# Kernel tuning notes

Hardware: AMD Instinct MI355X
Metric: run time of the kernel (lower is better)

## Reference

```python
import jax, jax.numpy as jnp
import numpy as np

B, N, IN_F = 2, 512, 10
SET_FEATS = [128, 128, 64]
HIDDEN = 256
D2 = 2 * SET_FEATS[-1]


def _init_linear(key, fout, fin):
    kw, kb = jax.random.split(key)
    bound = 1.0 / np.sqrt(fin)
    W = jax.random.uniform(kw, (fout, fin), jnp.float32, -bound, bound)
    b = jax.random.uniform(kb, (fout,), jnp.float32, -bound, bound)
    return W, b


def setup_inputs() -> dict:
    key = jax.random.key(0)
    keys = jax.random.split(key, 6)
    x = jax.random.normal(keys[0], (B, N, IN_F), jnp.float32)
    Ws0, bs0 = _init_linear(keys[1], SET_FEATS[0], IN_F)
    Ws1, bs1 = _init_linear(keys[2], SET_FEATS[1], SET_FEATS[0])
    Ws2, bs2 = _init_linear(keys[3], SET_FEATS[2], SET_FEATS[1])
    Wp0, bp0 = _init_linear(keys[4], HIDDEN, D2)
    Wp1, bp1 = _init_linear(keys[5], 1, HIDDEN)
    return {"x": x, "Ws0": Ws0, "bs0": bs0, "Ws1": Ws1, "bs1": bs1,
            "Ws2": Ws2, "bs2": bs2, "Wp0": Wp0, "bp0": bp0,
            "Wp1": Wp1, "bp1": bp1}


def reference(x, Ws0, bs0, Ws1, bs1, Ws2, bs2, Wp0, bp0, Wp1, bp1):
    # x: [B, N, in_features] -> transpose(2,1) -> [B, C, N]
    u = jnp.transpose(x, (0, 2, 1))
    # set_model: per-point MLP (1x1 conv stack), ReLU after each layer
    for W, b in ((Ws0, bs0), (Ws1, bs1), (Ws2, bs2)):
        u = jax.nn.relu(jnp.einsum('fc,bcn->bfn', W, u) + b[None, :, None])
    # pairwise block: cat([u_j broadcast, u_i broadcast], dim=1) -> [B, 2d, N, N]
    # fused into the first suffix 1x1 conv: out[b,f,i,j] = Wa@u[:,j] + Wb@u[:,i] + b
    d = Wp0.shape[1] // 2
    Wa, Wb = Wp0[:, :d], Wp0[:, d:]
    ha = jnp.einsum('fc,bcn->bfn', Wa, u)  # depends on j (m1[b,c,i,j] = u[b,c,j])
    hb = jnp.einsum('fc,bcn->bfn', Wb, u)  # depends on i (m2[b,c,i,j] = u[b,c,i])
    h = jax.nn.relu(ha[:, :, None, :] + hb[:, :, :, None] + bp0[None, :, None, None])
    # final 1x1 conv to 1 channel, no activation
    out = jnp.einsum('fc,bcij->bfij', Wp1, h) + bp1[None, :, None, None]
    return out  # [B, 1, N, N]
```

## Files before the change

kernel.cpp:

```cpp
#include <hip/hip_runtime.h>

#define BB 2
#define NN 512
#define INF 10
#define TI 64
#define TJ 32
#define FCH 128

static __device__ __forceinline__ float dot4(float4 w, float4 v, float acc) {
    acc = fmaf(w.x, v.x, acc);
    acc = fmaf(w.y, v.y, acc);
    acc = fmaf(w.z, v.z, acc);
    acc = fmaf(w.w, v.w, acc);
    return acc;
}

__global__ __launch_bounds__(256) void k_points(
    const float* __restrict__ x,
    const float* __restrict__ Ws0, const float* __restrict__ bs0,
    const float* __restrict__ Ws1, const float* __restrict__ bs1,
    const float* __restrict__ Ws2, const float* __restrict__ bs2,
    const float* __restrict__ Wp0, const float* __restrict__ bp0,
    float* __restrict__ haT, float* __restrict__ hbT)
{
    __shared__ __align__(16) float xs[4][INF];
    __shared__ __align__(16) float u0s[4][128];
    __shared__ __align__(16) float u1s[4][128];
    __shared__ __align__(16) float u2s[4][64];

    const int t  = threadIdx.x;
    const int p0 = blockIdx.x * 4;

    if (t < 4 * INF) {
        int p = t / INF, c = t % INF;
        xs[p][c] = x[(p0 + p) * INF + c];
    }
    __syncthreads();

    {
        const int f = t & 127, ph = t >> 7;
        float a0 = bs0[f], a1 = a0;
        #pragma unroll
        for (int c = 0; c < INF; ++c) {
            float w = Ws0[f * INF + c];
            a0 = fmaf(w, xs[ph * 2 + 0][c], a0);
            a1 = fmaf(w, xs[ph * 2 + 1][c], a1);
        }
        u0s[ph * 2 + 0][f] = fmaxf(a0, 0.f);
        u0s[ph * 2 + 1][f] = fmaxf(a1, 0.f);
    }
    __syncthreads();

    {
        const int f = t & 127, ph = t >> 7;
        float a0 = bs1[f], a1 = a0;
        const float4* wv = (const float4*)(Ws1 + f * 128);
        #pragma unroll 8
        for (int c4 = 0; c4 < 32; ++c4) {
            float4 w  = wv[c4];
            float4 x0 = *(const float4*)&u0s[ph * 2 + 0][c4 * 4];
            float4 x1 = *(const float4*)&u0s[ph * 2 + 1][c4 * 4];
            a0 = dot4(w, x0, a0);
            a1 = dot4(w, x1, a1);
        }
        u1s[ph * 2 + 0][f] = fmaxf(a0, 0.f);
        u1s[ph * 2 + 1][f] = fmaxf(a1, 0.f);
    }
    __syncthreads();

    {
        const int f = t & 63, p = t >> 6;
        float a = bs2[f];
        const float4* wv = (const float4*)(Ws2 + f * 128);
        #pragma unroll 8
        for (int c4 = 0; c4 < 32; ++c4) {
            float4 w  = wv[c4];
            float4 xv = *(const float4*)&u1s[p][c4 * 4];
            a = dot4(w, xv, a);
        }
        u2s[p][f] = fmaxf(a, 0.f);
    }
    __syncthreads();

    {
        const int f = t;
        float ah[4], bh[4];
        const float bb = bp0[f];
        #pragma unroll
        for (int p = 0; p < 4; ++p) { ah[p] = 0.f; bh[p] = bb; }
        const float4* wv = (const float4*)(Wp0 + f * 128);
        #pragma unroll 4
        for (int c4 = 0; c4 < 16; ++c4) {
            float4 wa = wv[c4];
            float4 wb = wv[16 + c4];
            #pragma unroll
            for (int p = 0; p < 4; ++p) {
                float4 u = *(const float4*)&u2s[p][c4 * 4];
                ah[p] = dot4(wa, u, ah[p]);
                bh[p] = dot4(wb, u, bh[p]);
            }
        }
        #pragma unroll
        for (int p = 0; p < 4; ++p) {
            haT[(size_t)(p0 + p) * 256 + f] = ah[p];
            hbT[(size_t)(p0 + p) * 256 + f] = bh[p];
        }
    }
}

__global__ __launch_bounds__(256) void k_outer(
    const float* __restrict__ haT, const float* __restrict__ hbT,
    const float* __restrict__ Wp1, const float* __restrict__ bp1,
    float* __restrict__ out)
{
    __shared__ __align__(512) float sA[TJ * FCH];
    __shared__ __align__(512) float sB[TI * FCH];

    const int t  = threadIdx.x;
    const int jb = blockIdx.x * TJ;
    const int ib = blockIdx.y * TI;
    const int b  = blockIdx.z;

    const int lane = t & 63, w = t >> 6;
    const int lj = lane & 15;
    const int li = lane >> 4;
    const int j0 = lj * 2;
    const int i0 = w * 16 + li * 4;
    const int xa = lj;
    const int xb = w * 4 + li;

    const uintptr_t aB0 = (uintptr_t)sA + (size_t)j0 * (FCH * 4) + (xa << 4);
    const uintptr_t aB1 = aB0 + FCH * 4;
    uintptr_t bBs[4];
    #pragma unroll
    for (int di = 0; di < 4; ++di)
        bBs[di] = (uintptr_t)sB + (size_t)(i0 + di) * (FCH * 4) + (xb << 4);

    float acc[4][2];
    #pragma unroll
    for (int di = 0; di < 4; ++di) { acc[di][0] = 0.f; acc[di][1] = 0.f; }

    const int sp = t & 31;

    for (int ph = 0; ph < 2; ++ph) {
        const int f0 = ph * FCH;
        if (ph) __syncthreads();

        #pragma unroll
        for (int k = 0; k < 4; ++k) {
            const int r  = (t >> 5) + 8 * k;
            const int sg = sp ^ ((r >> 1) & 15);
            float4 v = *(const float4*)(haT + ((size_t)(b * NN + jb + r)) * 256 + f0 + sg * 4);
            *(float4*)&sA[r * FCH + sp * 4] = v;
        }
        #pragma unroll
        for (int k = 0; k < 8; ++k) {
            const int r  = (t >> 5) + 8 * k;
            const int sg = sp ^ ((r >> 2) & 15);
            float4 v = *(const float4*)(hbT + ((size_t)(b * NN + ib + r)) * 256 + f0 + sg * 4);
            *(float4*)&sB[r * FCH + sp * 4] = v;
        }
        __syncthreads();

        const float4* wg = (const float4*)(Wp1 + f0);

        #pragma unroll 8
        for (int g = 0; g < 32; ++g) {
            const float4 w4 = wg[g];
            const uintptr_t gx = (uintptr_t)(g << 4);
            const float4 a0 = *(const float4*)(aB0 ^ gx);
            const float4 a1 = *(const float4*)(aB1 ^ gx);
            float4 bv[4];
            #pragma unroll
            for (int di = 0; di < 4; ++di) bv[di] = *(const float4*)(bBs[di] ^ gx);

            #pragma unroll
            for (int di = 0; di < 4; ++di) {
                acc[di][0] = fmaf(w4.x, fmaxf(a0.x + bv[di].x, 0.f), acc[di][0]);
                acc[di][1] = fmaf(w4.x, fmaxf(a1.x + bv[di].x, 0.f), acc[di][1]);
                acc[di][0] = fmaf(w4.y, fmaxf(a0.y + bv[di].y, 0.f), acc[di][0]);
                acc[di][1] = fmaf(w4.y, fmaxf(a1.y + bv[di].y, 0.f), acc[di][1]);
                acc[di][0] = fmaf(w4.z, fmaxf(a0.z + bv[di].z, 0.f), acc[di][0]);
                acc[di][1] = fmaf(w4.z, fmaxf(a1.z + bv[di].z, 0.f), acc[di][1]);
                acc[di][0] = fmaf(w4.w, fmaxf(a0.w + bv[di].w, 0.f), acc[di][0]);
                acc[di][1] = fmaf(w4.w, fmaxf(a1.w + bv[di].w, 0.f), acc[di][1]);
            }
        }
    }

    const float bias = bp1[0];
    float* o = out + (size_t)b * NN * NN;
    #pragma unroll
    for (int di = 0; di < 4; ++di) {
        float2 v = { acc[di][0] + bias, acc[di][1] + bias };
        *(float2*)&o[(size_t)(ib + i0 + di) * NN + (jb + j0)] = v;
    }
}

extern "C" void kernel_launch(void* const* d_in, const int* in_sizes, int n_in,
                              void* d_out, int out_size, void* d_ws, size_t ws_size,
                              hipStream_t stream) {
    const float* x   = (const float*)d_in[0];
    const float* Ws0 = (const float*)d_in[1];
    const float* bs0 = (const float*)d_in[2];
    const float* Ws1 = (const float*)d_in[3];
    const float* bs1 = (const float*)d_in[4];
    const float* Ws2 = (const float*)d_in[5];
    const float* bs2 = (const float*)d_in[6];
    const float* Wp0 = (const float*)d_in[7];
    const float* bp0 = (const float*)d_in[8];
    const float* Wp1 = (const float*)d_in[9];
    const float* bp1 = (const float*)d_in[10];

    float* haT = (float*)d_ws;
    float* hbT = haT + (size_t)BB * NN * 256;

    k_points<<<dim3(BB * NN / 4), dim3(256), 0, stream>>>(
        x, Ws0, bs0, Ws1, bs1, Ws2, bs2, Wp0, bp0, haT, hbT);

    k_outer<<<dim3(NN / TJ, NN / TI, BB), dim3(256), 0, stream>>>(
        haT, hbT, Wp1, bp1, (float*)d_out);
}
```

Before: 108.7 us.

## Prefetch second feature half into registers and use index-based swizzled LDS addressing

```diff
diff --git a/kernel.cpp b/kernel.cpp
--- a/kernel.cpp
+++ b/kernel.cpp
@@ -129,50 +129,59 @@
     const int xa = lj;
     const int xb = w * 4 + li;
 
-    const uintptr_t aB0 = (uintptr_t)sA + (size_t)j0 * (FCH * 4) + (xa << 4);
-    const uintptr_t aB1 = aB0 + FCH * 4;
-    uintptr_t bBs[4];
-    #pragma unroll
-    for (int di = 0; di < 4; ++di)
-        bBs[di] = (uintptr_t)sB + (size_t)(i0 + di) * (FCH * 4) + (xb << 4);
+    const int aOff0 = j0 * FCH;
+    const int aOff1 = aOff0 + FCH;
+    const int bOff0 = i0 * FCH;
 
     float acc[4][2];
     #pragma unroll
     for (int di = 0; di < 4; ++di) { acc[di][0] = 0.f; acc[di][1] = 0.f; }
 
     const int sp = t & 31;
-
-    for (int ph = 0; ph < 2; ++ph) {
-        const int f0 = ph * FCH;
-        if (ph) __syncthreads();
-
-        #pragma unroll
-        for (int k = 0; k < 4; ++k) {
-            const int r  = (t >> 5) + 8 * k;
-            const int sg = sp ^ ((r >> 1) & 15);
-            float4 v = *(const float4*)(haT + ((size_t)(b * NN + jb + r)) * 256 + f0 + sg * 4);
-            *(float4*)&sA[r * FCH + sp * 4] = v;
-        }
-        #pragma unroll
-        for (int k = 0; k < 8; ++k) {
-            const int r  = (t >> 5) + 8 * k;
-            const int sg = sp ^ ((r >> 2) & 15);
-            float4 v = *(const float4*)(hbT + ((size_t)(b * NN + ib + r)) * 256 + f0 + sg * 4);
-            *(float4*)&sB[r * FCH + sp * 4] = v;
-        }
-        __syncthreads();
-
-        const float4* wg = (const float4*)(Wp1 + f0);
-
+    const int sr = t >> 5;
+
+    #pragma unroll
+    for (int k = 0; k < 4; ++k) {
+        const int r  = sr + 8 * k;
+        const int sg = sp ^ ((r >> 1) & 15);
+        float4 v = *(const float4*)(haT + ((size_t)(b * NN + jb + r)) * 256 + sg * 4);
+        *(float4*)&sA[r * FCH + sp * 4] = v;
+    }
+    #pragma unroll
+    for (int k = 0; k < 8; ++k) {
+        const int r  = sr + 8 * k;
+        const int sg = sp ^ ((r >> 2) & 15);
+        float4 v = *(const float4*)(hbT + ((size_t)(b * NN + ib + r)) * 256 + sg * 4);
+        *(float4*)&sB[r * FCH + sp * 4] = v;
+    }
+    __syncthreads();
+
+    float4 pfA[4], pfB[8];
+    #pragma unroll
+    for (int k = 0; k < 4; ++k) {
+        const int r  = sr + 8 * k;
+        const int sg = sp ^ ((r >> 1) & 15);
+        pfA[k] = *(const float4*)(haT + ((size_t)(b * NN + jb + r)) * 256 + FCH + sg * 4);
+    }
+    #pragma unroll
+    for (int k = 0; k < 8; ++k) {
+        const int r  = sr + 8 * k;
+        const int sg = sp ^ ((r >> 2) & 15);
+        pfB[k] = *(const float4*)(hbT + ((size_t)(b * NN + ib + r)) * 256 + FCH + sg * 4);
+    }
+
+    auto compute = [&](const float4* wg) {
         #pragma unroll 8
         for (int g = 0; g < 32; ++g) {
             const float4 w4 = wg[g];
-            const uintptr_t gx = (uintptr_t)(g << 4);
-            const float4 a0 = *(const float4*)(aB0 ^ gx);
-            const float4 a1 = *(const float4*)(aB1 ^ gx);
+            const int ga = (g ^ xa) << 2;
+            const int gb = (g ^ xb) << 2;
+            const float4 a0 = *(const float4*)&sA[aOff0 + ga];
+            const float4 a1 = *(const float4*)&sA[aOff1 + ga];
             float4 bv[4];
             #pragma unroll
-            for (int di = 0; di < 4; ++di) bv[di] = *(const float4*)(bBs[di] ^ gx);
+            for (int di = 0; di < 4; ++di)
+                bv[di] = *(const float4*)&sB[bOff0 + di * FCH + gb];
 
             #pragma unroll
             for (int di = 0; di < 4; ++di) {
@@ -186,7 +195,24 @@
                 acc[di][1] = fmaf(w4.w, fmaxf(a1.w + bv[di].w, 0.f), acc[di][1]);
             }
         }
-    }
+    };
+
+    compute((const float4*)Wp1);
+    __syncthreads();
+
+    #pragma unroll
+    for (int k = 0; k < 4; ++k) {
+        const int r = sr + 8 * k;
+        *(float4*)&sA[r * FCH + sp * 4] = pfA[k];
+    }
+    #pragma unroll
+    for (int k = 0; k < 8; ++k) {
+        const int r = sr + 8 * k;
+        *(float4*)&sB[r * FCH + sp * 4] = pfB[k];
+    }
+    __syncthreads();
+
+    compute((const float4*)(Wp1 + FCH));
 
     const float bias = bp1[0];
     float* o = out + (size_t)b * NN * NN;
```

Result: slower. 112.3 us (+3.3%).
